# Kernel tuning notes

Measured on AMD Instinct MI355X. Metric: run time of the kernel, lower is better.

## Reference

```python
import jax, jax.numpy as jnp
import numpy as np

N = 1024      # num_features
H = 256       # num_hidden_features
E = 64        # embedding_size
HD = 64       # hidden_size
B = 8192


def setup_inputs() -> dict:
    key = jax.random.key(0)
    ks = jax.random.split(key, 7)
    glorot_e = (2.0 / (N + E)) ** 0.5
    glorot_w = (2.0 / (2 * E + HD)) ** 0.5
    glorot_u = (2.0 / (HD + 1)) ** 0.5
    return {
        "values": jax.random.uniform(ks[0], (B, N), dtype=jnp.float32),
        "feat_emb": jax.random.normal(ks[1], (N, E), dtype=jnp.float32) * glorot_e,
        "hid_emb": jax.random.normal(ks[2], (H, E), dtype=jnp.float32) * glorot_e,
        "W_w": jax.random.normal(ks[3], (2 * E, HD), dtype=jnp.float32) * glorot_w,
        "b_w": jnp.zeros((HD,), dtype=jnp.float32),
        "W_u": jax.random.normal(ks[4], (HD, 1), dtype=jnp.float32) * glorot_u,
        "mask": jax.random.bernoulli(ks[5], 0.5, (N, N + H)),
    }


def _forward(values, feat_emb, hid_emb, W_w, b_w, W_u, mask):
    # full embedding table over extended vocab: [M, E], M = N + H
    full = jnp.concatenate([feat_emb, hid_emb], axis=0)
    # Dense w applied to concat([feat_i, full_j]) == split-matmul, avoids [N,M,2E]
    W1, W2 = W_w[:E], W_w[E:]                      # each [E, HD]
    a = feat_emb @ W1                              # [N, HD]
    b = full @ W2                                  # [M, HD]
    h = jnp.tanh(a[:, None, :] + b[None, :, :] + b_w)  # [N, M, HD]
    score = jnp.squeeze(h @ W_u, axis=-1)          # [N, M]
    score = jnp.where(mask, jnp.exp(score), 0.0)
    score_sum = jnp.sum(score, axis=1, keepdims=True)
    score_sum = jnp.where(score_sum == 0, 1.0, score_sum)
    attention_weights = score / score_sum          # [N, M]
    context = attention_weights @ full             # [N, E]
    return values @ context                        # [B, E]


def reference(values, feat_emb, hid_emb, W_w, b_w, W_u, mask):
    return _forward(values, feat_emb, hid_emb, W_w, b_w, W_u, mask)
```

## Files before the change

kernel.cpp:

```cpp
#include <hip/hip_runtime.h>
#include <hip/hip_bf16.h>

#define NF   1024
#define NHID 256
#define NJ   1280
#define ED   64
#define BATCH 8192
#define SCB  640

#if defined(__has_builtin) && __has_builtin(__builtin_amdgcn_exp2f)
#define EXP2(x) __builtin_amdgcn_exp2f(x)
#else
#define EXP2(x) exp2f(x)
#endif
#define K2E 2.8853900817779268f

__global__ __launch_bounds__(256) void prep_kernel(
    const float* __restrict__ feat, const float* __restrict__ hid,
    const float* __restrict__ Ww, const float* __restrict__ bw,
    float* __restrict__ A, float* __restrict__ BvT)
{
    __shared__ __align__(16) float in_s[64][64];
    __shared__ __align__(16) float tout[64][65];
    const int tid = threadIdx.x;
    const int b   = blockIdx.x;
    const bool isA = (b < 16);
    const int e  = tid & 63;
    const int wv = tid >> 6;

    const float* W = isA ? Ww : (Ww + 4096);
    float wcol[64];
    #pragma unroll
    for (int k = 0; k < 64; k++) wcol[k] = W[k * 64 + e];
    const float bias = isA ? 0.f : bw[e];

    const int bb = isA ? b : (b - 16);
    const float* src = isA ? (feat + (size_t)bb * 4096)
                     : (bb < 16 ? (feat + (size_t)bb * 4096)
                                : (hid + (size_t)(bb - 16) * 4096));
    #pragma unroll
    for (int s = 0; s < 4; s++)
        ((float4*)&in_s[0][0])[tid + s * 256] = ((const float4*)src)[tid + s * 256];
    __syncthreads();

    float acc[16];
    #pragma unroll
    for (int r = 0; r < 16; r++) acc[r] = bias;
    for (int k4 = 0; k4 < 64; k4 += 4) {
        #pragma unroll
        for (int r = 0; r < 16; r++) {
            float4 iv = *(const float4*)&in_s[wv * 16 + r][k4];
            acc[r] += iv.x*wcol[k4+0] + iv.y*wcol[k4+1] + iv.z*wcol[k4+2] + iv.w*wcol[k4+3];
        }
    }

    if (isA) {
        #pragma unroll
        for (int r = 0; r < 16; r++)
            A[(size_t)(b * 64 + wv * 16 + r) * 64 + e] = acc[r];
    } else {
        #pragma unroll
        for (int r = 0; r < 16; r++) tout[wv * 16 + r][e] = acc[r];
        __syncthreads();
        const int j0 = bb * 64;
        #pragma unroll
        for (int q = 0; q < 4; q++) {
            float4 v;
            v.x = tout[wv * 16 + q * 4 + 0][e];
            v.y = tout[wv * 16 + q * 4 + 1][e];
            v.z = tout[wv * 16 + q * 4 + 2][e];
            v.w = tout[wv * 16 + q * 4 + 3][e];
            *(float4*)&BvT[(size_t)e * NJ + j0 + wv * 16 + q * 4] = v;
        }
    }
}

__global__ __launch_bounds__(SCB) void score_ctx_kernel(
    const float* __restrict__ feat, const float* __restrict__ hid,
    const float* __restrict__ Wu, const float* __restrict__ A,
    const float* __restrict__ BvT, const void* __restrict__ maskp,
    float* __restrict__ ctx)
{
    __shared__ __align__(16) float4 sA4[64];
    __shared__ __align__(16) float  sWu[64];
    __shared__ __align__(16) float  sc[4][NJ];
    __shared__ __align__(16) float  red[4][40][64];
    __shared__ float wpart[4][10];
    __shared__ float ssum[4];
    __shared__ float sSwu;
    __shared__ int   mtype_s;

    const int tid = threadIdx.x;
    const int i0  = blockIdx.x * 4;

    if (tid < 64) {
        const unsigned int* mw = (const unsigned int*)maskp;
        unsigned int w = mw[tid];
        unsigned long long notf = __ballot(w != 0u && w != 0x3F800000u);
        unsigned long long gt1  = __ballot(w > 1u);
        if (tid == 0) mtype_s = (notf == 0ull) ? 2 : ((gt1 == 0ull) ? 1 : 0);
        float wu = Wu[tid];
        float4 p;
        p.x = A[(size_t)(i0 + 0) * 64 + tid];
        p.y = A[(size_t)(i0 + 1) * 64 + tid];
        p.z = A[(size_t)(i0 + 2) * 64 + tid];
        p.w = A[(size_t)(i0 + 3) * 64 + tid];
        sA4[tid] = p;
        sWu[tid] = wu;
        float s = wu;
        #pragma unroll
        for (int off = 32; off > 0; off >>= 1) s += __shfl_down(s, off);
        if (tid == 0) sSwu = s;
    }
    __syncthreads();

    const int j2 = tid * 2;
    float2 acc[4];
    #pragma unroll
    for (int i = 0; i < 4; i++) acc[i] = make_float2(0.f, 0.f);

    #pragma unroll 4
    for (int e = 0; e < 64; e++) {
        float2 b = *(const float2*)(BvT + (size_t)e * NJ + j2);
        float4 p = sA4[e];
        float wu = sWu[e];
        float x, r;
        x = p.x + b.x; r = __builtin_amdgcn_rcpf(EXP2(x*K2E) + 1.f); acc[0].x = fmaf(wu, r, acc[0].x);
        x = p.x + b.y; r = __builtin_amdgcn_rcpf(EXP2(x*K2E) + 1.f); acc[0].y = fmaf(wu, r, acc[0].y);
        x = p.y + b.x; r = __builtin_amdgcn_rcpf(EXP2(x*K2E) + 1.f); acc[1].x = fmaf(wu, r, acc[1].x);
        x = p.y + b.y; r = __builtin_amdgcn_rcpf(EXP2(x*K2E) + 1.f); acc[1].y = fmaf(wu, r, acc[1].y);
        x = p.z + b.x; r = __builtin_amdgcn_rcpf(EXP2(x*K2E) + 1.f); acc[2].x = fmaf(wu, r, acc[2].x);
        x = p.z + b.y; r = __builtin_amdgcn_rcpf(EXP2(x*K2E) + 1.f); acc[2].y = fmaf(wu, r, acc[2].y);
        x = p.w + b.x; r = __builtin_amdgcn_rcpf(EXP2(x*K2E) + 1.f); acc[3].x = fmaf(wu, r, acc[3].x);
        x = p.w + b.y; r = __builtin_amdgcn_rcpf(EXP2(x*K2E) + 1.f); acc[3].y = fmaf(wu, r, acc[3].y);
    }

    const float Swu = sSwu;
    const int mtype = mtype_s;
    const unsigned char* m8  = (const unsigned char*)maskp;
    const unsigned int*  m32 = (const unsigned int*)maskp;
    const float*         mfl = (const float*)maskp;

    float lsum[4];
    #pragma unroll
    for (int i = 0; i < 4; i++) {
        size_t off = (size_t)(i0 + i) * NJ + j2;
        bool b0, b1;
        if (mtype == 0) {
            unsigned short m = *(const unsigned short*)(m8 + off);
            b0 = (m & 0xffu) != 0; b1 = (m >> 8) != 0;
        } else if (mtype == 1) {
            uint2 m = *(const uint2*)(m32 + off);
            b0 = m.x != 0u; b1 = m.y != 0u;
        } else {
            float2 m = *(const float2*)(mfl + off);
            b0 = m.x != 0.f; b1 = m.y != 0.f;
        }
        float e0 = b0 ? __expf(Swu - 2.f * acc[i].x) : 0.f;
        float e1 = b1 ? __expf(Swu - 2.f * acc[i].y) : 0.f;
        *(float2*)&sc[i][j2] = make_float2(e0, e1);
        lsum[i] = e0 + e1;
    }
    #pragma unroll
    for (int off = 32; off > 0; off >>= 1) {
        lsum[0] += __shfl_down(lsum[0], off);
        lsum[1] += __shfl_down(lsum[1], off);
        lsum[2] += __shfl_down(lsum[2], off);
        lsum[3] += __shfl_down(lsum[3], off);
    }
    if ((tid & 63) == 0) {
        int wv = tid >> 6;
        wpart[0][wv] = lsum[0]; wpart[1][wv] = lsum[1];
        wpart[2][wv] = lsum[2]; wpart[3][wv] = lsum[3];
    }
    __syncthreads();
    if (tid < 4) {
        float s = 0.f;
        #pragma unroll
        for (int g = 0; g < 10; g++) s += wpart[tid][g];
        ssum[tid] = (s == 0.f) ? 1.f : s;
    }
    __syncthreads();

    const int jg = tid >> 4;
    const int e4 = (tid & 15) * 4;
    float4 c[4];
    #pragma unroll
    for (int i = 0; i < 4; i++) c[i] = make_float4(0.f, 0.f, 0.f, 0.f);
    for (int it = 0; it < 32; it++) {
        int j = it * 40 + jg;
        const float* fr = (j < NF) ? (feat + (size_t)j * 64)
                                   : (hid  + (size_t)(j - NF) * 64);
        float4 f = *(const float4*)(fr + e4);
        #pragma unroll
        for (int i = 0; i < 4; i++) {
            float w = sc[i][j];
            c[i].x += w*f.x; c[i].y += w*f.y; c[i].z += w*f.z; c[i].w += w*f.w;
        }
    }
    #pragma unroll
    for (int i = 0; i < 4; i++) *(float4*)&red[i][jg][e4] = c[i];
    __syncthreads();
    if (tid < 256) {
        int half = tid >> 6, e = tid & 63;
        float v = 0.f;
        #pragma unroll
        for (int g = 0; g < 40; g++) v += red[half][g][e];
        ctx[(size_t)(i0 + half) * 64 + e] = v / ssum[half];
    }
}

__global__ __launch_bounds__(256) void out_mm_kernel(
    const float* __restrict__ values, const float* __restrict__ ctxp,
    float* __restrict__ dst, int atomic_mode)
{
    __shared__ __align__(16) float vsT[64 * 64];
    __shared__ __align__(16) float cs[64][64];
    const int tid = threadIdx.x;
    const int rt  = blockIdx.x >> 3;
    const int kq  = blockIdx.x & 7;
    const int r0  = rt * 64;
    const int tr  = tid >> 4;
    const int tc4 = (tid & 15) * 4;

    float acc[4][4];
    #pragma unroll
    for (int a = 0; a < 4; a++)
        #pragma unroll
        for (int b = 0; b < 4; b++) acc[a][b] = 0.f;

    for (int ch = 0; ch < 2; ch++) {
        const int k0 = kq * 128 + ch * 64;
        __syncthreads();
        #pragma unroll
        for (int s = 0; s < 4; s++) {
            int t   = tid + s * 256;
            int r   = t >> 4;
            int kk4 = (t & 15) * 4;
            float4 g = *(const float4*)&values[(size_t)(r0 + r) * NF + k0 + kk4];
            int p  = (((r >> 2) + (t & 15)) & 15) * 4 + (r & 3);
            vsT[(kk4 + 0) * 64 + p] = g.x;
            vsT[(kk4 + 1) * 64 + p] = g.y;
            vsT[(kk4 + 2) * 64 + p] = g.z;
            vsT[(kk4 + 3) * 64 + p] = g.w;
        }
        #pragma unroll
        for (int s = 0; s < 4; s++) {
            int t  = tid + s * 256;
            int kk = t >> 4;
            int c4 = (t & 15) * 4;
            *(float4*)&cs[kk][c4] = *(const float4*)&ctxp[(size_t)(k0 + kk) * ED + c4];
        }
        __syncthreads();
        #pragma unroll 8
        for (int k = 0; k < 64; k++) {
            float4 av = *(const float4*)&vsT[k * 64 + (((tr + (k >> 2)) & 15) << 2)];
            float4 bv = *(const float4*)&cs[k][tc4];
            acc[0][0] += av.x*bv.x; acc[0][1] += av.x*bv.y; acc[0][2] += av.x*bv.z; acc[0][3] += av.x*bv.w;
            acc[1][0] += av.y*bv.x; acc[1][1] += av.y*bv.y; acc[1][2] += av.y*bv.z; acc[1][3] += av.y*bv.w;
            acc[2][0] += av.z*bv.x; acc[2][1] += av.z*bv.y; acc[2][2] += av.z*bv.z; acc[2][3] += av.z*bv.w;
            acc[3][0] += av.w*bv.x; acc[3][1] += av.w*bv.y; acc[3][2] += av.w*bv.z; acc[3][3] += av.w*bv.w;
        }
    }
    if (atomic_mode) {
        #pragma unroll
        for (int i2 = 0; i2 < 4; i2++) {
            int r = r0 + tr * 4 + i2;
            float* op = dst + (size_t)r * ED + tc4;
            unsafeAtomicAdd(op + 0, acc[i2][0]);
            unsafeAtomicAdd(op + 1, acc[i2][1]);
            unsafeAtomicAdd(op + 2, acc[i2][2]);
            unsafeAtomicAdd(op + 3, acc[i2][3]);
        }
    } else {
        #pragma unroll
        for (int i2 = 0; i2 < 4; i2++) {
            int r = r0 + tr * 4 + i2;
            float* op = dst + ((size_t)kq * BATCH + r) * ED + tc4;
            *(float4*)op = make_float4(acc[i2][0], acc[i2][1], acc[i2][2], acc[i2][3]);
        }
    }
}

__global__ __launch_bounds__(256) void reduce8_kernel(
    const float* __restrict__ part, float* __restrict__ out)
{
    const size_t S = (size_t)BATCH * ED / 4;
    size_t idx = (size_t)blockIdx.x * 256 + threadIdx.x;
    const float4* p = (const float4*)part;
    float4 r = {0.f, 0.f, 0.f, 0.f};
    #pragma unroll
    for (int q = 0; q < 8; q++) {
        float4 a = p[idx + (size_t)q * S];
        r.x += a.x; r.y += a.y; r.z += a.z; r.w += a.w;
    }
    ((float4*)out)[idx] = r;
}

extern "C" void kernel_launch(void* const* d_in, const int* in_sizes, int n_in,
                              void* d_out, int out_size, void* d_ws, size_t ws_size,
                              hipStream_t stream) {
    const float* values = (const float*)d_in[0];
    const float* feat   = (const float*)d_in[1];
    const float* hid    = (const float*)d_in[2];
    const float* Ww     = (const float*)d_in[3];
    const float* bw     = (const float*)d_in[4];
    const float* Wu     = (const float*)d_in[5];
    const void*  mask   = d_in[6];
    float* out = (float*)d_out;

    float* A    = (float*)d_ws;
    float* BvT  = A + (size_t)NF * 64;
    float* ctx  = BvT + (size_t)ED * NJ;
    float* part = ctx + (size_t)NF * 64;
    const size_t need = ((size_t)NF*64 + (size_t)ED*NJ + (size_t)NF*64
                         + (size_t)8*BATCH*ED) * sizeof(float);
    const bool wsmode = ws_size >= need;

    hipLaunchKernelGGL(prep_kernel, dim3(36), dim3(256), 0, stream,
                       feat, hid, Ww, bw, A, BvT);
    hipLaunchKernelGGL(score_ctx_kernel, dim3(NF / 4), dim3(SCB), 0, stream,
                       feat, hid, Wu, A, BvT, mask, ctx);
    if (wsmode) {
        hipLaunchKernelGGL(out_mm_kernel, dim3(1024), dim3(256), 0, stream,
                           values, ctx, part, 0);
        hipLaunchKernelGGL(reduce8_kernel, dim3(BATCH * ED / 4 / 256), dim3(256), 0, stream,
                           part, out);
    } else {
        hipMemsetAsync(d_out, 0, (size_t)BATCH * ED * sizeof(float), stream);
        hipLaunchKernelGGL(out_mm_kernel, dim3(1024), dim3(256), 0, stream,
                           values, ctx, out, 1);
    }
}
```

Before: 172.9 us.

## Split score and context kernels, enlarge output GEMM tiles, drop partial reduce

The fused score/context kernel is split in two. A score kernel over 512 blocks writes the masked exponentials to global memory, and a separate ctx kernel reloads them, normalises and multiplies by the embeddings. The exp2 scale constants are folded into the prep outputs and Wu, and exp2 is emitted through inline v_exp_f32. The output GEMM now uses 128-row tiles with an 8x8 register block and a swizzled LDS transpose, and accumulates with atomics into a zeroed output instead of writing partials that a separate reduce kernel summed. The score split adds global traffic and an extra launch, while the atomics replace the reduce pass.

```diff
diff --git a/kernel.cpp b/kernel.cpp
--- a/kernel.cpp
+++ b/kernel.cpp
@@ -6,19 +6,20 @@
 #define NJ   1280
 #define ED   64
 #define BATCH 8192
-#define SCB  640
-
-#if defined(__has_builtin) && __has_builtin(__builtin_amdgcn_exp2f)
-#define EXP2(x) __builtin_amdgcn_exp2f(x)
-#else
-#define EXP2(x) exp2f(x)
-#endif
-#define K2E 2.8853900817779268f
+
+#define K2E   2.8853900817779268f
+#define LOG2E 1.4426950408889634f
+
+__device__ __forceinline__ float exp2_fast(float x) {
+    float r;
+    asm volatile("v_exp_f32 %0, %1" : "=v"(r) : "v"(x));
+    return r;
+}
 
 __global__ __launch_bounds__(256) void prep_kernel(
     const float* __restrict__ feat, const float* __restrict__ hid,
     const float* __restrict__ Ww, const float* __restrict__ bw,
-    float* __restrict__ A, float* __restrict__ BvT)
+    float* __restrict__ Ap, float* __restrict__ BvT)
 {
     __shared__ __align__(16) float in_s[64][64];
     __shared__ __align__(16) float tout[64][65];
@@ -57,10 +58,10 @@
     if (isA) {
         #pragma unroll
         for (int r = 0; r < 16; r++)
-            A[(size_t)(b * 64 + wv * 16 + r) * 64 + e] = acc[r];
+            Ap[(size_t)(b * 64 + wv * 16 + r) * 64 + e] = acc[r] * K2E;
     } else {
         #pragma unroll
-        for (int r = 0; r < 16; r++) tout[wv * 16 + r][e] = acc[r];
+        for (int r = 0; r < 16; r++) tout[wv * 16 + r][e] = acc[r] * K2E;
         __syncthreads();
         const int j0 = bb * 64;
         #pragma unroll
@@ -75,23 +76,19 @@
     }
 }
 
-__global__ __launch_bounds__(SCB) void score_ctx_kernel(
-    const float* __restrict__ feat, const float* __restrict__ hid,
-    const float* __restrict__ Wu, const float* __restrict__ A,
+__global__ __launch_bounds__(320) void score_kernel(
+    const float* __restrict__ Wu, const float* __restrict__ Ap,
     const float* __restrict__ BvT, const void* __restrict__ maskp,
-    float* __restrict__ ctx)
+    float* __restrict__ sc)
 {
     __shared__ __align__(16) float4 sA4[64];
-    __shared__ __align__(16) float  sWu[64];
-    __shared__ __align__(16) float  sc[4][NJ];
-    __shared__ __align__(16) float  red[4][40][64];
-    __shared__ float wpart[4][10];
-    __shared__ float ssum[4];
-    __shared__ float sSwu;
+    __shared__ float sWu2[64];
+    __shared__ float sSwuL;
     __shared__ int   mtype_s;
 
     const int tid = threadIdx.x;
-    const int i0  = blockIdx.x * 4;
+    const int i0  = (blockIdx.x >> 1) * 4;
+    const int j0  = (blockIdx.x & 1) * 640;
 
     if (tid < 64) {
         const unsigned int* mw = (const unsigned int*)maskp;
@@ -101,20 +98,20 @@
         if (tid == 0) mtype_s = (notf == 0ull) ? 2 : ((gt1 == 0ull) ? 1 : 0);
         float wu = Wu[tid];
         float4 p;
-        p.x = A[(size_t)(i0 + 0) * 64 + tid];
-        p.y = A[(size_t)(i0 + 1) * 64 + tid];
-        p.z = A[(size_t)(i0 + 2) * 64 + tid];
-        p.w = A[(size_t)(i0 + 3) * 64 + tid];
-        sA4[tid] = p;
-        sWu[tid] = wu;
+        p.x = Ap[(size_t)(i0 + 0) * 64 + tid];
+        p.y = Ap[(size_t)(i0 + 1) * 64 + tid];
+        p.z = Ap[(size_t)(i0 + 2) * 64 + tid];
+        p.w = Ap[(size_t)(i0 + 3) * 64 + tid];
+        sA4[tid]  = p;
+        sWu2[tid] = wu * (2.0f * LOG2E);
         float s = wu;
         #pragma unroll
         for (int off = 32; off > 0; off >>= 1) s += __shfl_down(s, off);
-        if (tid == 0) sSwu = s;
+        if (tid == 0) sSwuL = s * LOG2E;
     }
     __syncthreads();
 
-    const int j2 = tid * 2;
+    const int j2 = j0 + tid * 2;
     float2 acc[4];
     #pragma unroll
     for (int i = 0; i < 4; i++) acc[i] = make_float2(0.f, 0.f);
@@ -122,26 +119,25 @@
     #pragma unroll 4
     for (int e = 0; e < 64; e++) {
         float2 b = *(const float2*)(BvT + (size_t)e * NJ + j2);
-        float4 p = sA4[e];
-        float wu = sWu[e];
-        float x, r;
-        x = p.x + b.x; r = __builtin_amdgcn_rcpf(EXP2(x*K2E) + 1.f); acc[0].x = fmaf(wu, r, acc[0].x);
-        x = p.x + b.y; r = __builtin_amdgcn_rcpf(EXP2(x*K2E) + 1.f); acc[0].y = fmaf(wu, r, acc[0].y);
-        x = p.y + b.x; r = __builtin_amdgcn_rcpf(EXP2(x*K2E) + 1.f); acc[1].x = fmaf(wu, r, acc[1].x);
-        x = p.y + b.y; r = __builtin_amdgcn_rcpf(EXP2(x*K2E) + 1.f); acc[1].y = fmaf(wu, r, acc[1].y);
-        x = p.z + b.x; r = __builtin_amdgcn_rcpf(EXP2(x*K2E) + 1.f); acc[2].x = fmaf(wu, r, acc[2].x);
-        x = p.z + b.y; r = __builtin_amdgcn_rcpf(EXP2(x*K2E) + 1.f); acc[2].y = fmaf(wu, r, acc[2].y);
-        x = p.w + b.x; r = __builtin_amdgcn_rcpf(EXP2(x*K2E) + 1.f); acc[3].x = fmaf(wu, r, acc[3].x);
-        x = p.w + b.y; r = __builtin_amdgcn_rcpf(EXP2(x*K2E) + 1.f); acc[3].y = fmaf(wu, r, acc[3].y);
-    }
-
-    const float Swu = sSwu;
+        float4 a = sA4[e];
+        float w2 = sWu2[e];
+        float t, r;
+        t = a.x + b.x; r = __builtin_amdgcn_rcpf(exp2_fast(t) + 1.f); acc[0].x = fmaf(w2, r, acc[0].x);
+        t = a.x + b.y; r = __builtin_amdgcn_rcpf(exp2_fast(t) + 1.f); acc[0].y = fmaf(w2, r, acc[0].y);
+        t = a.y + b.x; r = __builtin_amdgcn_rcpf(exp2_fast(t) + 1.f); acc[1].x = fmaf(w2, r, acc[1].x);
+        t = a.y + b.y; r = __builtin_amdgcn_rcpf(exp2_fast(t) + 1.f); acc[1].y = fmaf(w2, r, acc[1].y);
+        t = a.z + b.x; r = __builtin_amdgcn_rcpf(exp2_fast(t) + 1.f); acc[2].x = fmaf(w2, r, acc[2].x);
+        t = a.z + b.y; r = __builtin_amdgcn_rcpf(exp2_fast(t) + 1.f); acc[2].y = fmaf(w2, r, acc[2].y);
+        t = a.w + b.x; r = __builtin_amdgcn_rcpf(exp2_fast(t) + 1.f); acc[3].x = fmaf(w2, r, acc[3].x);
+        t = a.w + b.y; r = __builtin_amdgcn_rcpf(exp2_fast(t) + 1.f); acc[3].y = fmaf(w2, r, acc[3].y);
+    }
+
+    const float SwuL = sSwuL;
     const int mtype = mtype_s;
     const unsigned char* m8  = (const unsigned char*)maskp;
     const unsigned int*  m32 = (const unsigned int*)maskp;
     const float*         mfl = (const float*)maskp;
 
-    float lsum[4];
     #pragma unroll
     for (int i = 0; i < 4; i++) {
         size_t off = (size_t)(i0 + i) * NJ + j2;
@@ -156,145 +152,136 @@
             float2 m = *(const float2*)(mfl + off);
             b0 = m.x != 0.f; b1 = m.y != 0.f;
         }
-        float e0 = b0 ? __expf(Swu - 2.f * acc[i].x) : 0.f;
-        float e1 = b1 ? __expf(Swu - 2.f * acc[i].y) : 0.f;
-        *(float2*)&sc[i][j2] = make_float2(e0, e1);
-        lsum[i] = e0 + e1;
-    }
-    #pragma unroll
-    for (int off = 32; off > 0; off >>= 1) {
-        lsum[0] += __shfl_down(lsum[0], off);
-        lsum[1] += __shfl_down(lsum[1], off);
-        lsum[2] += __shfl_down(lsum[2], off);
-        lsum[3] += __shfl_down(lsum[3], off);
-    }
-    if ((tid & 63) == 0) {
-        int wv = tid >> 6;
-        wpart[0][wv] = lsum[0]; wpart[1][wv] = lsum[1];
-        wpart[2][wv] = lsum[2]; wpart[3][wv] = lsum[3];
+        float e0 = b0 ? exp2_fast(SwuL - acc[i].x) : 0.f;
+        float e1 = b1 ? exp2_fast(SwuL - acc[i].y) : 0.f;
+        *(float2*)&sc[off] = make_float2(e0, e1);
+    }
+}
+
+__global__ __launch_bounds__(256) void ctx_kernel(
+    const float* __restrict__ feat, const float* __restrict__ hid,
+    const float* __restrict__ sc, float* __restrict__ ctx)
+{
+    __shared__ __align__(16) float sc_s[4][NJ];
+    __shared__ __align__(16) float red[4][16][64];
+    __shared__ float ssum_s[4];
+    const int tid = threadIdx.x;
+    const int i0  = blockIdx.x * 4;
+
+    #pragma unroll
+    for (int rep = 0; rep < 5; rep++) {
+        int idx = tid + rep * 256;
+        int i   = idx / 320;
+        int jq  = idx - i * 320;
+        *(float4*)&sc_s[i][jq * 4] = *(const float4*)&sc[(size_t)(i0 + i) * NJ + jq * 4];
     }
     __syncthreads();
-    if (tid < 4) {
+    {
+        int i = tid >> 6, e = tid & 63;
         float s = 0.f;
         #pragma unroll
-        for (int g = 0; g < 10; g++) s += wpart[tid][g];
-        ssum[tid] = (s == 0.f) ? 1.f : s;
-    }
-    __syncthreads();
+        for (int g = 0; g < 20; g++) s += sc_s[i][e + g * 64];
+        #pragma unroll
+        for (int off = 32; off > 0; off >>= 1) s += __shfl_down(s, off);
+        if (e == 0) ssum_s[i] = (s == 0.f) ? 1.f : s;
+    }
 
     const int jg = tid >> 4;
     const int e4 = (tid & 15) * 4;
     float4 c[4];
     #pragma unroll
     for (int i = 0; i < 4; i++) c[i] = make_float4(0.f, 0.f, 0.f, 0.f);
-    for (int it = 0; it < 32; it++) {
-        int j = it * 40 + jg;
+    for (int it = 0; it < 80; it++) {
+        int j = it * 16 + jg;
         const float* fr = (j < NF) ? (feat + (size_t)j * 64)
                                    : (hid  + (size_t)(j - NF) * 64);
         float4 f = *(const float4*)(fr + e4);
         #pragma unroll
         for (int i = 0; i < 4; i++) {
-            float w = sc[i][j];
+            float w = sc_s[i][j];
             c[i].x += w*f.x; c[i].y += w*f.y; c[i].z += w*f.z; c[i].w += w*f.w;
         }
     }
     #pragma unroll
     for (int i = 0; i < 4; i++) *(float4*)&red[i][jg][e4] = c[i];
     __syncthreads();
-    if (tid < 256) {
+    {
         int half = tid >> 6, e = tid & 63;
         float v = 0.f;
         #pragma unroll
-        for (int g = 0; g < 40; g++) v += red[half][g][e];
-        ctx[(size_t)(i0 + half) * 64 + e] = v / ssum[half];
-    }
-}
-
-__global__ __launch_bounds__(256) void out_mm_kernel(
+        for (int g = 0; g < 16; g++) v += red[half][g][e];
+        ctx[(size_t)(i0 + half) * 64 + e] = v / ssum_s[half];
+    }
+}
+
+__global__ __launch_bounds__(128) void out_mm_kernel(
     const float* __restrict__ values, const float* __restrict__ ctxp,
-    float* __restrict__ dst, int atomic_mode)
+    float* __restrict__ out)
 {
-    __shared__ __align__(16) float vsT[64 * 64];
+    __shared__ __align__(16) float vsT[64 * 128];
     __shared__ __align__(16) float cs[64][64];
     const int tid = threadIdx.x;
     const int rt  = blockIdx.x >> 3;
     const int kq  = blockIdx.x & 7;
-    const int r0  = rt * 64;
-    const int tr  = tid >> 4;
-    const int tc4 = (tid & 15) * 4;
-
-    float acc[4][4];
-    #pragma unroll
-    for (int a = 0; a < 4; a++)
-        #pragma unroll
-        for (int b = 0; b < 4; b++) acc[a][b] = 0.f;
-
-    for (int ch = 0; ch < 2; ch++) {
-        const int k0 = kq * 128 + ch * 64;
+    const int r0  = rt * 128;
+    const int trg8 = (tid >> 3) * 8;
+    const int tc8  = (tid & 7) * 8;
+
+    float acc[8][8];
+    #pragma unroll
+    for (int a = 0; a < 8; a++)
+        #pragma unroll
+        for (int b = 0; b < 8; b++) acc[a][b] = 0.f;
+
+    for (int kt = 0; kt < 2; kt++) {
+        const int k0 = kq * 128 + kt * 64;
         __syncthreads();
         #pragma unroll
-        for (int s = 0; s < 4; s++) {
-            int t   = tid + s * 256;
-            int r   = t >> 4;
-            int kk4 = (t & 15) * 4;
-            float4 g = *(const float4*)&values[(size_t)(r0 + r) * NF + k0 + kk4];
-            int p  = (((r >> 2) + (t & 15)) & 15) * 4 + (r & 3);
-            vsT[(kk4 + 0) * 64 + p] = g.x;
-            vsT[(kk4 + 1) * 64 + p] = g.y;
-            vsT[(kk4 + 2) * 64 + p] = g.z;
-            vsT[(kk4 + 3) * 64 + p] = g.w;
-        }
-        #pragma unroll
-        for (int s = 0; s < 4; s++) {
-            int t  = tid + s * 256;
+        for (int s = 0; s < 16; s++) {
+            int t  = tid + s * 128;
+            int r  = t >> 4;
+            int k4 = (t & 15) * 4;
+            float4 g = *(const float4*)&values[(size_t)(r0 + r) * NF + k0 + k4];
+            #pragma unroll
+            for (int q = 0; q < 4; q++) {
+                int k = k4 + q;
+                int swz = ((k >> 2) & 3) << 3;
+                float gv = (q == 0) ? g.x : (q == 1) ? g.y : (q == 2) ? g.z : g.w;
+                vsT[k * 128 + (r ^ swz)] = gv;
+            }
+        }
+        #pragma unroll
+        for (int s = 0; s < 8; s++) {
+            int t  = tid + s * 128;
             int kk = t >> 4;
             int c4 = (t & 15) * 4;
             *(float4*)&cs[kk][c4] = *(const float4*)&ctxp[(size_t)(k0 + kk) * ED + c4];
         }
         __syncthreads();
-        #pragma unroll 8
+        #pragma unroll 4
         for (int k = 0; k < 64; k++) {
-            float4 av = *(const float4*)&vsT[k * 64 + (((tr + (k >> 2)) & 15) << 2)];
-            float4 bv = *(const float4*)&cs[k][tc4];
-            acc[0][0] += av.x*bv.x; acc[0][1] += av.x*bv.y; acc[0][2] += av.x*bv.z; acc[0][3] += av.x*bv.w;
-            acc[1][0] += av.y*bv.x; acc[1][1] += av.y*bv.y; acc[1][2] += av.y*bv.z; acc[1][3] += av.y*bv.w;
-            acc[2][0] += av.z*bv.x; acc[2][1] += av.z*bv.y; acc[2][2] += av.z*bv.z; acc[2][3] += av.z*bv.w;
-            acc[3][0] += av.w*bv.x; acc[3][1] += av.w*bv.y; acc[3][2] += av.w*bv.z; acc[3][3] += av.w*bv.w;
-        }
-    }
-    if (atomic_mode) {
-        #pragma unroll
-        for (int i2 = 0; i2 < 4; i2++) {
-            int r = r0 + tr * 4 + i2;
-            float* op = dst + (size_t)r * ED + tc4;
-            unsafeAtomicAdd(op + 0, acc[i2][0]);
-            unsafeAtomicAdd(op + 1, acc[i2][1]);
-            unsafeAtomicAdd(op + 2, acc[i2][2]);
-            unsafeAtomicAdd(op + 3, acc[i2][3]);
-        }
-    } else {
-        #pragma unroll
-        for (int i2 = 0; i2 < 4; i2++) {
-            int r = r0 + tr * 4 + i2;
-            float* op = dst + ((size_t)kq * BATCH + r) * ED + tc4;
-            *(float4*)op = make_float4(acc[i2][0], acc[i2][1], acc[i2][2], acc[i2][3]);
-        }
-    }
-}
-
-__global__ __launch_bounds__(256) void reduce8_kernel(
-    const float* __restrict__ part, float* __restrict__ out)
-{
-    const size_t S = (size_t)BATCH * ED / 4;
-    size_t idx = (size_t)blockIdx.x * 256 + threadIdx.x;
-    const float4* p = (const float4*)part;
-    float4 r = {0.f, 0.f, 0.f, 0.f};
-    #pragma unroll
-    for (int q = 0; q < 8; q++) {
-        float4 a = p[idx + (size_t)q * S];
-        r.x += a.x; r.y += a.y; r.z += a.z; r.w += a.w;
-    }
-    ((float4*)out)[idx] = r;
+            int swz = ((k >> 2) & 3) << 3;
+            int abase = k * 128 + (trg8 ^ swz);
+            float4 a0 = *(const float4*)&vsT[abase];
+            float4 a1 = *(const float4*)&vsT[abase + 4];
+            float4 b0 = *(const float4*)&cs[k][tc8];
+            float4 b1 = *(const float4*)&cs[k][tc8 + 4];
+            float av[8] = {a0.x,a0.y,a0.z,a0.w,a1.x,a1.y,a1.z,a1.w};
+            float bv[8] = {b0.x,b0.y,b0.z,b0.w,b1.x,b1.y,b1.z,b1.w};
+            #pragma unroll
+            for (int ri = 0; ri < 8; ri++)
+                #pragma unroll
+                for (int ci = 0; ci < 8; ci++)
+                    acc[ri][ci] += av[ri] * bv[ci];
+        }
+    }
+    #pragma unroll
+    for (int ri = 0; ri < 8; ri++) {
+        float* op = out + (size_t)(r0 + trg8 + ri) * ED + tc8;
+        #pragma unroll
+        for (int ci = 0; ci < 8; ci++)
+            unsafeAtomicAdd(op + ci, acc[ri][ci]);
+    }
 }
 
 extern "C" void kernel_launch(void* const* d_in, const int* in_sizes, int n_in,
@@ -309,26 +296,18 @@
     const void*  mask   = d_in[6];
     float* out = (float*)d_out;
 
-    float* A    = (float*)d_ws;
-    float* BvT  = A + (size_t)NF * 64;
-    float* ctx  = BvT + (size_t)ED * NJ;
-    float* part = ctx + (size_t)NF * 64;
-    const size_t need = ((size_t)NF*64 + (size_t)ED*NJ + (size_t)NF*64
-                         + (size_t)8*BATCH*ED) * sizeof(float);
-    const bool wsmode = ws_size >= need;
-
+    float* Ap  = (float*)d_ws;
+    float* BvT = Ap + (size_t)NF * 64;
+    float* ctx = BvT + (size_t)ED * NJ;
+    float* sc  = ctx + (size_t)NF * 64;
+
+    hipMemsetAsync(d_out, 0, (size_t)BATCH * ED * sizeof(float), stream);
     hipLaunchKernelGGL(prep_kernel, dim3(36), dim3(256), 0, stream,
-                       feat, hid, Ww, bw, A, BvT);
-    hipLaunchKernelGGL(score_ctx_kernel, dim3(NF / 4), dim3(SCB), 0, stream,
-                       feat, hid, Wu, A, BvT, mask, ctx);
-    if (wsmode) {
-        hipLaunchKernelGGL(out_mm_kernel, dim3(1024), dim3(256), 0, stream,
-                           values, ctx, part, 0);
-        hipLaunchKernelGGL(reduce8_kernel, dim3(BATCH * ED / 4 / 256), dim3(256), 0, stream,
-                           part, out);
-    } else {
-        hipMemsetAsync(d_out, 0, (size_t)BATCH * ED * sizeof(float), stream);
-        hipLaunchKernelGGL(out_mm_kernel, dim3(1024), dim3(256), 0, stream,
-                           values, ctx, out, 1);
-    }
-}
+                       feat, hid, Ww, bw, Ap, BvT);
+    hipLaunchKernelGGL(score_kernel, dim3(512), dim3(320), 0, stream,
+                       Wu, Ap, BvT, mask, sc);
+    hipLaunchKernelGGL(ctx_kernel, dim3(256), dim3(256), 0, stream,
+                       feat, hid, sc, ctx);
+    hipLaunchKernelGGL(out_mm_kernel, dim3(512), dim3(128), 0, stream,
+                       values, ctx, out);
+}
```

Result: slower. 267.7 us (+54.9%).
